# Performance work log

Measured on AMD Instinct MI355X. Metric: run time of the kernel, lower is better.

Reference implementation:

```python
import jax, jax.numpy as jnp
import numpy as np
import math

EMBED_DIM = 1024
N_HEAD = 16
HEAD_DIM = EMBED_DIM // N_HEAD


def setup_inputs() -> dict:
    key = jax.random.key(0)
    ks = jax.random.split(key, 9)
    B, T, C = 4, 2048, EMBED_DIM
    s = 1.0 / math.sqrt(C)
    return {
        "x": jax.random.normal(ks[0], (B, T, C), dtype=jnp.float32),
        "Wq": jax.random.normal(ks[1], (C, C), dtype=jnp.float32) * s,
        "bq": jnp.zeros((C,), dtype=jnp.float32),
        "Wk": jax.random.normal(ks[2], (C, C), dtype=jnp.float32) * s,
        "bk": jnp.zeros((C,), dtype=jnp.float32),
        "Wv": jax.random.normal(ks[3], (C, C), dtype=jnp.float32) * s,
        "bv": jnp.zeros((C,), dtype=jnp.float32),
        "Wp": jax.random.normal(ks[4], (C, C), dtype=jnp.float32) * s,
        "bp": jnp.zeros((C,), dtype=jnp.float32),
    }


def reference(x, Wq, bq, Wk, bk, Wv, bv, Wp, bp):
    B, T, C = x.shape
    H, D = N_HEAD, HEAD_DIM

    def heads(W, b):
        # [B,T,C] -> [B,H,T,D]
        return (x @ W.T + b).reshape(B, T, H, D).transpose(0, 2, 1, 3)

    q = heads(Wq, bq)
    k = heads(Wk, bk)
    v = heads(Wv, bv)

    att = jnp.einsum("bhtd,bhsd->bhts", q, k) * (1.0 / math.sqrt(D))
    causal = jnp.tril(jnp.ones((T, T), dtype=bool))
    att = jnp.where(causal[None, None], att, -jnp.inf)
    att = jax.nn.softmax(att, axis=-1)
    y = jnp.einsum("bhts,bhsd->bhtd", att, v)  # [B,H,T,D]
    y = y.transpose(0, 2, 1, 3).reshape(B, T, C)
    return y @ Wp.T + bp
```

## Files before the change

### kernel.cpp

```cpp
#include <hip/hip_runtime.h>
#include <hip/hip_bf16.h>
#include <cstdint>
#include <cstddef>

#define TQ 2048
#define CDIM 1024
#define NH 16
#define HD 64

typedef __attribute__((ext_vector_type(8))) short bf16x8;
typedef __attribute__((ext_vector_type(4))) float f32x4;
typedef __attribute__((ext_vector_type(16))) float f32x16;

__device__ __forceinline__ unsigned short f2bf(float f) {
  union { float f; unsigned u; } x; x.f = f;
  unsigned r = x.u + 0x7fffu + ((x.u >> 16) & 1u);
  return (unsigned short)(r >> 16);
}

__device__ __forceinline__ unsigned cvtpk(float lo, float hi) {
  unsigned r;
  asm("v_cvt_pk_bf16_f32 %0, %1, %2" : "=v"(r) : "v"(lo), "v"(hi));
  return r;
}

__device__ __forceinline__ void plswap(unsigned& x, unsigned& y) {
  asm("v_permlane32_swap_b32 %0, %1" : "+v"(x), "+v"(y));
}

__device__ __forceinline__ float exp2_fast(float x) {
  float r;
  asm("v_exp_f32 %0, %1" : "=v"(r) : "v"(x));
  return r;
}

__device__ __forceinline__ void gload_lds16(const void* g, void* l) {
  typedef __attribute__((address_space(1))) const void gv;
  typedef __attribute__((address_space(3))) void lv;
  __builtin_amdgcn_global_load_lds((gv*)g, (lv*)l, 16, 0, 0);
}

#define BAR() do { asm volatile("" ::: "memory"); __builtin_amdgcn_s_barrier(); asm volatile("" ::: "memory"); } while (0)
#define VMC2() asm volatile("s_waitcnt vmcnt(2)" ::: "memory")
#define VMC0() asm volatile("s_waitcnt vmcnt(0)" ::: "memory")

__global__ void cvt_bf16_kernel(const float* __restrict__ in,
                                unsigned short* __restrict__ out, int n) {
  int stride = gridDim.x * blockDim.x;
  for (int i = blockIdx.x * blockDim.x + threadIdx.x; i * 4 < n; i += stride) {
    float4 v = *(const float4*)(in + (size_t)i * 4);
    ushort4 o;
    o.x = f2bf(v.x); o.y = f2bf(v.y); o.z = f2bf(v.z); o.w = f2bf(v.w);
    *(ushort4*)(out + (size_t)i * 4) = o;
  }
}

__global__ void cvt4_kernel(const float* __restrict__ w0, const float* __restrict__ w1,
                            const float* __restrict__ w2, const float* __restrict__ w3,
                            unsigned short* __restrict__ out) {
  int i = blockIdx.x * blockDim.x + threadIdx.x;
  int which = i >> 18;
  const float* src = which == 0 ? w0 : which == 1 ? w1 : which == 2 ? w2 : w3;
  int off = (i & 262143) * 4;
  float4 v = *(const float4*)(src + off);
  ushort4 o;
  o.x = f2bf(v.x); o.y = f2bf(v.y); o.z = f2bf(v.z); o.w = f2bf(v.w);
  *(ushort4*)(out + (size_t)i * 4) = o;
}

template <int EPI>
__global__ __launch_bounds__(512, 2) void gemm256_kernel(
    const unsigned short* __restrict__ A,
    const unsigned short* __restrict__ Bt,
    const float* __restrict__ b0, const float* __restrict__ b1,
    void* __restrict__ outp,
    int M, int N, int K) {
  __shared__ __align__(16) char lds[131072];

  const int tid = (int)threadIdx.x;
  const int w = tid >> 6, lane = tid & 63;
  const int g = lane >> 4, c = lane & 15;
  const int wm = w >> 2, wn = w & 3;

  const int nbm = M >> 8, nbn = N >> 8;
  const int nwg = nbm * nbn;
  int id = (int)blockIdx.x;
  const int cpx = nwg >> 3;
  id = (id & 7) * cpx + (id >> 3);
  const int tm = id % nbm, tn = id / nbm;

  const char* Ab = (const char*)(A + (size_t)tm * 256 * K);
  const char* Bb = (const char*)(Bt + (size_t)tn * 256 * K);
  const int rowB = K * 2;
  const int nht = (K >> 6) << 2;

  char* aw = lds + wm * 16384;
  char* bw = lds + 65536 + (wn >> 1) * 16384;
  const int bfo = (wn & 1) * 8;

  auto stage_ht = [&](int j) {
    if (j >= nht) return;
    const int t = j >> 2, part = j & 3;
    const int isB = part >> 1, half = part & 1;
    const char* src = isB ? Bb : Ab;
    char* dst = lds + isB * 65536 + (t & 1) * 32768 + half * 16384 + w * 2048;
#pragma unroll
    for (int r = 0; r < 2; ++r) {
      const int f = w * 2 + r;
      const int m16 = f >> 1, ki = f & 1;
      gload_lds16(src + (size_t)(half * 128 + m16 * 16 + c) * rowB +
                      t * 128 + ki * 64 + g * 16,
                  dst + r * 1024);
    }
  };

  f32x4 acc[8][4];
#pragma unroll
  for (int i = 0; i < 8; ++i)
#pragma unroll
    for (int j = 0; j < 4; ++j) acc[i][j] = (f32x4){0.f, 0.f, 0.f, 0.f};
  bf16x8 af[4][2], bv[2][2];

  auto rdA = [&](int buf, int ms) {
#pragma unroll
    for (int mi = 0; mi < 4; ++mi)
#pragma unroll
      for (int ki = 0; ki < 2; ++ki)
        af[mi][ki] = *(const bf16x8*)(aw + buf * 32768 +
                                      ((ms * 4 + mi) * 2 + ki) * 1024 + lane * 16);
  };
  auto rdB = [&](int buf, int ns) {
#pragma unroll
    for (int ni = 0; ni < 2; ++ni)
#pragma unroll
      for (int ki = 0; ki < 2; ++ki)
        bv[ni][ki] = *(const bf16x8*)(bw + buf * 32768 +
                                      (bfo + (ns * 2 + ni) * 2 + ki) * 1024 + lane * 16);
  };
  auto mm = [&](int ms, int ns) {
    __builtin_amdgcn_s_setprio(1);
#pragma unroll
    for (int mi = 0; mi < 4; ++mi)
#pragma unroll
      for (int ni = 0; ni < 2; ++ni)
#pragma unroll
        for (int ki = 0; ki < 2; ++ki)
          acc[ms * 4 + mi][ns * 2 + ni] = __builtin_amdgcn_mfma_f32_16x16x32_bf16(
              af[mi][ki], bv[ni][ki], acc[ms * 4 + mi][ns * 2 + ni], 0, 0, 0);
    __builtin_amdgcn_s_setprio(0);
  };

  for (int j = 0; j < 5; ++j) stage_ht(j);
  VMC2();
  BAR();

  const int niter = K >> 7;
#pragma unroll 1
  for (int i = 0; i < niter; ++i) {
    const int j0 = 5 + (i << 3);
    rdA(0, 0); rdB(0, 0); stage_ht(j0 + 0); BAR(); mm(0, 0); BAR();
    rdB(0, 1);            stage_ht(j0 + 1); BAR(); mm(0, 1); BAR();
    rdA(0, 1);            stage_ht(j0 + 2); BAR(); mm(1, 1); BAR();
    rdB(0, 0);            stage_ht(j0 + 3);
    if (i + 1 < niter) { VMC2(); } else { VMC0(); }
    BAR(); mm(1, 0); BAR();
    rdA(1, 0); rdB(1, 0); stage_ht(j0 + 4); BAR(); mm(0, 0); BAR();
    rdB(1, 1);            stage_ht(j0 + 5); BAR(); mm(0, 1); BAR();
    rdA(1, 1);            stage_ht(j0 + 6); BAR(); mm(1, 1); BAR();
    rdB(1, 0);            stage_ht(j0 + 7); VMC2(); BAR(); mm(1, 0); BAR();
  }

#pragma unroll
  for (int mi = 0; mi < 8; ++mi) {
#pragma unroll
    for (int ni = 0; ni < 4; ++ni) {
      const int n = tn * 256 + wn * 64 + ni * 16 + c;
#pragma unroll
      for (int e = 0; e < 4; ++e) {
        const int m = tm * 256 + wm * 128 + mi * 16 + g * 4 + e;
        float v = acc[mi][ni][e];
        if (EPI == 4) {
          unsigned short* O = (unsigned short*)outp;
          if (n < 1024) {
            v = (v + b0[n]) * 0.18033688f;
            size_t idx = ((size_t)(m >> 11) * NH + (n >> 6)) * (TQ * HD) +
                         (size_t)(m & (TQ - 1)) * HD + (n & (HD - 1));
            O[idx] = f2bf(v);
          } else {
            int nn = n - 1024;
            v += b1[nn];
            size_t idx = 8388608 + ((size_t)(m >> 11) * NH + (nn >> 6)) * (TQ * HD) +
                         (size_t)(m & (TQ - 1)) * HD + (nn & (HD - 1));
            O[idx] = f2bf(v);
          }
        }
      }
    }
  }
}

template <int EPI>
__global__ __launch_bounds__(512, 2) void gemm128x256_kernel(
    const unsigned short* __restrict__ A,
    const unsigned short* __restrict__ Bt,
    const float* __restrict__ b0, const float* __restrict__ b1,
    void* __restrict__ outp,
    int M, int N, int K) {
  __shared__ __align__(16) char lds[98304];

  const int tid = (int)threadIdx.x;
  const int w = tid >> 6, lane = tid & 63;
  const int g = lane >> 4, c = lane & 15;
  const int wm = w >> 2, wn = w & 3;

  const int nbm = M >> 7, nbn = N >> 8;
  const int nwg = nbm * nbn;
  int id = (int)blockIdx.x;
  const int cpx = nwg >> 3;
  id = (id & 7) * cpx + (id >> 3);
  const int tm = id % nbm, tn = id / nbm;

  const char* Ab = (const char*)(A + (size_t)tm * 128 * K);
  const char* Bb = (const char*)(Bt + (size_t)tn * 256 * K);
  const int rowB = K * 2;
  const int nt = K >> 6;

  auto stageA = [&](int t) {
    if (t >= nt) return;
    char* dst = lds + (t & 1) * 49152 + (w << 11);
    const char* s = Ab + (size_t)(w * 16 + c) * rowB + t * 128 + g * 16;
    gload_lds16(s, dst);
    gload_lds16(s + 64, dst + 1024);
  };
  auto stageB = [&](int t, int odd) {
    if (t >= nt) return;
    const int n16 = (w >> 1) * 4 + 2 * odd + (w & 1);
    char* dst = lds + (t & 1) * 49152 + 16384 + (n16 << 11);
    const char* s = Bb + (size_t)(n16 * 16 + c) * rowB + t * 128 + g * 16;
    gload_lds16(s, dst);
    gload_lds16(s + 64, dst + 1024);
  };

  f32x4 acc[4][4];
#pragma unroll
  for (int i = 0; i < 4; ++i)
#pragma unroll
    for (int j = 0; j < 4; ++j) acc[i][j] = (f32x4){0.f, 0.f, 0.f, 0.f};
  bf16x8 af[2][2], bv[2][2][2];

  auto rdA = [&](int cur, int ms) {
#pragma unroll
    for (int mi2 = 0; mi2 < 2; ++mi2)
#pragma unroll
      for (int ki = 0; ki < 2; ++ki)
        af[mi2][ki] = *(const bf16x8*)(lds + cur * 49152 +
            (((wm * 4 + ms * 2 + mi2) << 1) + ki) * 1024 + lane * 16);
  };
  auto rdB = [&](int cur, int ns) {
#pragma unroll
    for (int ni2 = 0; ni2 < 2; ++ni2)
#pragma unroll
      for (int ki = 0; ki < 2; ++ki)
        bv[ns][ni2][ki] = *(const bf16x8*)(lds + cur * 49152 + 16384 +
            (((wn * 4 + ns * 2 + ni2) << 1) + ki) * 1024 + lane * 16);
  };
  auto mm = [&](int ms, int ns) {
    __builtin_amdgcn_s_setprio(1);
#pragma unroll
    for (int mi2 = 0; mi2 < 2; ++mi2)
#pragma unroll
      for (int ni2 = 0; ni2 < 2; ++ni2)
#pragma unroll
        for (int ki = 0; ki < 2; ++ki)
          acc[ms * 2 + mi2][ns * 2 + ni2] = __builtin_amdgcn_mfma_f32_16x16x32_bf16(
              af[mi2][ki], bv[ns][ni2][ki], acc[ms * 2 + mi2][ns * 2 + ni2], 0, 0, 0);
    __builtin_amdgcn_s_setprio(0);
  };

  stageA(0); stageB(0, 0); stageB(0, 1);
  VMC2();
  BAR();

#pragma unroll 1
  for (int i = 0; i < (nt >> 1); ++i) {
    const int t0 = 2 * i, t1 = 2 * i + 1;
    rdA(0, 0); rdB(0, 0); stageA(t0 + 1);
    mm(0, 0); VMC2(); BAR();
    rdB(0, 1); stageB(t0 + 1, 0);
    mm(0, 1); BAR();
    rdA(0, 1); stageB(t0 + 1, 1);
    mm(1, 1); BAR();
    mm(1, 0); VMC2(); BAR();
    rdA(1, 0); rdB(1, 0); stageA(t1 + 1);
    mm(0, 0);
    if (t1 == nt - 1) { VMC0(); } else { VMC2(); }
    BAR();
    rdB(1, 1); stageB(t1 + 1, 0);
    mm(0, 1); BAR();
    rdA(1, 1); stageB(t1 + 1, 1);
    mm(1, 1); BAR();
    mm(1, 0); VMC2(); BAR();
  }

#pragma unroll
  for (int mi = 0; mi < 4; ++mi) {
#pragma unroll
    for (int ni = 0; ni < 4; ++ni) {
      const int n = tn * 256 + wn * 64 + ni * 16 + c;
#pragma unroll
      for (int e = 0; e < 4; ++e) {
        const int m = tm * 128 + wm * 64 + mi * 16 + g * 4 + e;
        float v = acc[mi][ni][e];
        if (EPI == 1) {
          v += b0[m];
          size_t idx = ((size_t)(n >> 11) * (NH * HD) + m) * TQ + (n & (TQ - 1));
          ((unsigned short*)outp)[idx] = f2bf(v);
        } else if (EPI == 2) {
          v += b0[n];
          ((float*)outp)[(size_t)m * N + n] = v;
        }
      }
    }
  }
}

__global__ __launch_bounds__(256, 4) void attn_kernel(
    const unsigned short* __restrict__ Q,
    const unsigned short* __restrict__ K,
    const unsigned short* __restrict__ Vt,
    unsigned short* __restrict__ Y) {
  __shared__ __align__(16) char Ks[2][8192];
  __shared__ __align__(16) char Vs[2][8192];

  const int tid = (int)threadIdx.x;
  const int w = tid >> 6, lane = tid & 63;
  const int l31 = lane & 31, hi = lane >> 5;

  const int n = (int)blockIdx.x;
  const int g = n & 255, k = n >> 8;
  const int bh = g >> 2;
  const int u = 2 * (g & 3) + (k >> 1);
  const int qt = (k & 1) ? (15 - u) : u;
  const int b = bh >> 4, h = bh & 15;

  const unsigned short* Qb = Q + (size_t)bh * TQ * HD;
  const char* Kb = (const char*)(K + (size_t)bh * TQ * HD);
  const char* Vb = (const char*)(Vt + (size_t)bh * HD * TQ);

  auto stage = [&](int buf, int kt) {
#pragma unroll
    for (int i = 0; i < 2; ++i) {
      const int s = i * 256 + tid;
      const int r32 = (s >> 8) * 32 + (s & 31);
      const int ck = ((s >> 6) & 3) * 32 + ((s >> 5) & 1) * 16;
      char* kdst = &Ks[buf][0] + i * 4096 + (w << 10);
      char* vdst = &Vs[buf][0] + i * 4096 + (w << 10);
      gload_lds16(Kb + (size_t)kt * 8192 + r32 * 128 + ck, kdst);
      gload_lds16(Vb + (size_t)r32 * 4096 + kt * 128 + ck, vdst);
    }
  };

  const int q0 = qt * 128 + w * 32;
  const int qg = q0 + l31;
  const int nkv = 2 * qt + 2;

  stage(0, 0);

  bf16x8 qf[4];
#pragma unroll
  for (int dk = 0; dk < 4; ++dk)
    qf[dk] = *(const bf16x8*)(Qb + (size_t)qg * HD + dk * 16 + hi * 8);

  f32x16 oac[2];
#pragma unroll
  for (int nb = 0; nb < 2; ++nb)
#pragma unroll
    for (int r = 0; r < 16; ++r) oac[nb][r] = 0.f;
  float mr = -3.0e38f, lr = 0.f;

  __syncthreads();

  for (int kt = 0; kt < nkv; ++kt) {
    const int cur = kt & 1;
    if (kt + 1 < nkv) stage(cur ^ 1, kt + 1);

    if (kt * 64 <= q0 + 31) {
      const char* Klane = &Ks[cur][0] + lane * 16;
      const char* Vlane = &Vs[cur][0] + lane * 16;

      f32x16 s0, s1;
#pragma unroll
      for (int r = 0; r < 16; ++r) { s0[r] = 0.f; s1[r] = 0.f; }
#pragma unroll
      for (int dk = 0; dk < 4; ++dk) {
        bf16x8 kf0 = *(const bf16x8*)(Klane + (dk << 10));
        bf16x8 kf1 = *(const bf16x8*)(Klane + ((4 + dk) << 10));
        s0 = __builtin_amdgcn_mfma_f32_32x32x16_bf16(kf0, qf[dk], s0, 0, 0, 0);
        s1 = __builtin_amdgcn_mfma_f32_32x32x16_bf16(kf1, qf[dk], s1, 0, 0, 0);
      }

      const bool maskT = (kt * 64 + 63 > q0);
      if (maskT) {
#pragma unroll
        for (int r = 0; r < 16; ++r) {
          int kv0 = kt * 64 + ((r & 3) + 8 * (r >> 2)) + 4 * hi;
          s0[r] = (kv0 <= qg) ? s0[r] : -3.0e38f;
          s1[r] = (kv0 + 32 <= qg) ? s1[r] : -3.0e38f;
        }
      }

      float mt_ = s0[0];
#pragma unroll
      for (int r = 1; r < 16; ++r) mt_ = fmaxf(mt_, s0[r]);
#pragma unroll
      for (int r = 0; r < 16; ++r) mt_ = fmaxf(mt_, s1[r]);
      mt_ = fmaxf(mt_, __shfl_xor(mt_, 32));

      if (!__all(mt_ - mr <= 8.0f)) {
        const float mn = fmaxf(mr, mt_);
        const float al = exp2_fast(mr - mn);
        mr = mn;
        lr *= al;
#pragma unroll
        for (int nb = 0; nb < 2; ++nb)
#pragma unroll
          for (int r = 0; r < 16; ++r) oac[nb][r] *= al;
      }

      float rs = 0.f;
#pragma unroll
      for (int r = 0; r < 16; ++r) { s0[r] = exp2_fast(s0[r] - mr); rs += s0[r]; }
#pragma unroll
      for (int r = 0; r < 16; ++r) { s1[r] = exp2_fast(s1[r] - mr); rs += s1[r]; }
      rs += __shfl_xor(rs, 32);
      lr += rs;

      bf16x8 pf[4];
      {
        unsigned a0 = cvtpk(s0[0], s0[1]), b0 = cvtpk(s0[2], s0[3]);
        unsigned c0 = cvtpk(s0[4], s0[5]), d0 = cvtpk(s0[6], s0[7]);
        plswap(a0, c0); plswap(b0, d0);
        unsigned a1 = cvtpk(s0[8], s0[9]), b1 = cvtpk(s0[10], s0[11]);
        unsigned c1 = cvtpk(s0[12], s0[13]), d1 = cvtpk(s0[14], s0[15]);
        plswap(a1, c1); plswap(b1, d1);
        unsigned a2 = cvtpk(s1[0], s1[1]), b2 = cvtpk(s1[2], s1[3]);
        unsigned c2 = cvtpk(s1[4], s1[5]), d2 = cvtpk(s1[6], s1[7]);
        plswap(a2, c2); plswap(b2, d2);
        unsigned a3 = cvtpk(s1[8], s1[9]), b3 = cvtpk(s1[10], s1[11]);
        unsigned c3 = cvtpk(s1[12], s1[13]), d3 = cvtpk(s1[14], s1[15]);
        plswap(a3, c3); plswap(b3, d3);
        union { unsigned u[4]; bf16x8 v; } t;
        t.u[0] = a0; t.u[1] = b0; t.u[2] = c0; t.u[3] = d0; pf[0] = t.v;
        t.u[0] = a1; t.u[1] = b1; t.u[2] = c1; t.u[3] = d1; pf[1] = t.v;
        t.u[0] = a2; t.u[1] = b2; t.u[2] = c2; t.u[3] = d2; pf[2] = t.v;
        t.u[0] = a3; t.u[1] = b3; t.u[2] = c3; t.u[3] = d3; pf[3] = t.v;
      }

#pragma unroll
      for (int nb = 0; nb < 2; ++nb)
#pragma unroll
        for (int ks = 0; ks < 4; ++ks) {
          bf16x8 vf = *(const bf16x8*)(Vlane + (((nb << 2) + ks) << 10));
          oac[nb] = __builtin_amdgcn_mfma_f32_32x32x16_bf16(vf, pf[ks], oac[nb], 0, 0, 0);
        }
    }
    __syncthreads();
  }

  float inv;
  asm("v_rcp_f32 %0, %1" : "=v"(inv) : "v"(lr));
  unsigned short* Yrow = Y + (size_t)(b * TQ + qg) * CDIM + h * 64;
#pragma unroll
  for (int nb = 0; nb < 2; ++nb)
#pragma unroll
    for (int j = 0; j < 8; ++j) {
      const int dbase = ((2 * j) & 3) + 8 * (j >> 1);
      unsigned lo = f2bf(oac[nb][2 * j] * inv);
      unsigned hi2 = f2bf(oac[nb][2 * j + 1] * inv);
      *(unsigned*)(Yrow + nb * 32 + dbase + 4 * hi) = lo | (hi2 << 16);
    }
}

extern "C" void kernel_launch(void* const* d_in, const int* in_sizes, int n_in,
                              void* d_out, int out_size, void* d_ws, size_t ws_size,
                              hipStream_t stream) {
  (void)in_sizes; (void)n_in; (void)out_size; (void)ws_size;
  const float* x  = (const float*)d_in[0];
  const float* Wq = (const float*)d_in[1];
  const float* bq = (const float*)d_in[2];
  const float* Wk = (const float*)d_in[3];
  const float* bk = (const float*)d_in[4];
  const float* Wv = (const float*)d_in[5];
  const float* bv = (const float*)d_in[6];
  const float* Wp = (const float*)d_in[7];
  const float* bp = (const float*)d_in[8];
  float* out = (float*)d_out;

  char* ws = (char*)d_ws;
  unsigned short* xb  = (unsigned short*)(ws + 0);
  unsigned short* wqb = (unsigned short*)(ws + 16777216);
  unsigned short* wvb = (unsigned short*)(ws + 20971520);
  unsigned short* wpb = (unsigned short*)(ws + 23068672);
  unsigned short* Qh  = (unsigned short*)(ws + 25165824);
  unsigned short* Kh  = (unsigned short*)(ws + 41943040);
  unsigned short* Vt  = (unsigned short*)(ws + 58720256);
  unsigned short* y   = (unsigned short*)(ws + 75497472);

  const int nx = 4 * TQ * CDIM;

  cvt_bf16_kernel<<<4096, 256, 0, stream>>>(x, xb, nx);
  cvt4_kernel<<<4096, 256, 0, stream>>>(Wq, Wk, Wv, Wp, wqb);

  gemm256_kernel<4><<<256, 512, 0, stream>>>(xb, wqb, bq, bk, Qh, 8192, 2048, 1024);
  gemm128x256_kernel<1><<<256, 512, 0, stream>>>(wvb, xb, bv, bv, Vt, 1024, 8192, 1024);

  attn_kernel<<<1024, 256, 0, stream>>>(Qh, Kh, Vt, y);

  gemm128x256_kernel<2><<<256, 512, 0, stream>>>(y, wpb, bp, bp, out, 8192, 1024, 1024);
}
```

Before: 199.1 us.

## Merge conversion kernels, reorder GEMM tile mapping, tune attention softmax reductions

Combines the input and weight bf16 conversion kernels into one launch to save a kernel launch. Changes the workgroup-to-tile mapping in the QK GEMM and the output projection GEMM to row-major order for better L2 reuse. In attention, raises wave priority around MFMA blocks, and replaces the serial max and sum reductions with v_max3-based and pairwise tree reductions to shorten dependency chains. These are several independent micro-optimizations, and the priority hints and tile-order changes may help or hurt depending on scheduling.

```diff
diff --git a/kernel.cpp b/kernel.cpp
--- a/kernel.cpp
+++ b/kernel.cpp
@@ -34,6 +34,12 @@
   return r;
 }
 
+__device__ __forceinline__ float fmax3(float a, float b, float c) {
+  float r;
+  asm("v_max3_f32 %0, %1, %2, %3" : "=v"(r) : "v"(a), "v"(b), "v"(c));
+  return r;
+}
+
 __device__ __forceinline__ void gload_lds16(const void* g, void* l) {
   typedef __attribute__((address_space(1))) const void gv;
   typedef __attribute__((address_space(3))) void lv;
@@ -44,28 +50,29 @@
 #define VMC2() asm volatile("s_waitcnt vmcnt(2)" ::: "memory")
 #define VMC0() asm volatile("s_waitcnt vmcnt(0)" ::: "memory")
 
-__global__ void cvt_bf16_kernel(const float* __restrict__ in,
-                                unsigned short* __restrict__ out, int n) {
-  int stride = gridDim.x * blockDim.x;
-  for (int i = blockIdx.x * blockDim.x + threadIdx.x; i * 4 < n; i += stride) {
-    float4 v = *(const float4*)(in + (size_t)i * 4);
+__global__ void cvt_all_kernel(const float* __restrict__ x,
+                               const float* __restrict__ w0, const float* __restrict__ w1,
+                               const float* __restrict__ w2, const float* __restrict__ w3,
+                               unsigned short* __restrict__ xb,
+                               unsigned short* __restrict__ wb) {
+  const int bid = (int)blockIdx.x;
+  if (bid < 4096) {
+    for (int i = bid * 256 + threadIdx.x; i < 2097152; i += 4096 * 256) {
+      float4 v = *(const float4*)(x + (size_t)i * 4);
+      ushort4 o;
+      o.x = f2bf(v.x); o.y = f2bf(v.y); o.z = f2bf(v.z); o.w = f2bf(v.w);
+      *(ushort4*)(xb + (size_t)i * 4) = o;
+    }
+  } else {
+    int i = (bid - 4096) * 256 + threadIdx.x;
+    int which = i >> 18;
+    const float* src = which == 0 ? w0 : which == 1 ? w1 : which == 2 ? w2 : w3;
+    int off = (i & 262143) * 4;
+    float4 v = *(const float4*)(src + off);
     ushort4 o;
     o.x = f2bf(v.x); o.y = f2bf(v.y); o.z = f2bf(v.z); o.w = f2bf(v.w);
-    *(ushort4*)(out + (size_t)i * 4) = o;
+    *(ushort4*)(wb + (size_t)i * 4) = o;
   }
-}
-
-__global__ void cvt4_kernel(const float* __restrict__ w0, const float* __restrict__ w1,
-                            const float* __restrict__ w2, const float* __restrict__ w3,
-                            unsigned short* __restrict__ out) {
-  int i = blockIdx.x * blockDim.x + threadIdx.x;
-  int which = i >> 18;
-  const float* src = which == 0 ? w0 : which == 1 ? w1 : which == 2 ? w2 : w3;
-  int off = (i & 262143) * 4;
-  float4 v = *(const float4*)(src + off);
-  ushort4 o;
-  o.x = f2bf(v.x); o.y = f2bf(v.y); o.z = f2bf(v.z); o.w = f2bf(v.w);
-  *(ushort4*)(out + (size_t)i * 4) = o;
 }
 
 template <int EPI>
@@ -87,7 +94,7 @@
   int id = (int)blockIdx.x;
   const int cpx = nwg >> 3;
   id = (id & 7) * cpx + (id >> 3);
-  const int tm = id % nbm, tn = id / nbm;
+  const int tn = id % nbn, tm = id / nbn;
 
   const char* Ab = (const char*)(A + (size_t)tm * 256 * K);
   const char* Bb = (const char*)(Bt + (size_t)tn * 256 * K);
@@ -199,7 +206,7 @@
   }
 }
 
-template <int EPI>
+template <int EPI, int ROWMAJ>
 __global__ __launch_bounds__(512, 2) void gemm128x256_kernel(
     const unsigned short* __restrict__ A,
     const unsigned short* __restrict__ Bt,
@@ -218,7 +225,8 @@
   int id = (int)blockIdx.x;
   const int cpx = nwg >> 3;
   id = (id & 7) * cpx + (id >> 3);
-  const int tm = id % nbm, tn = id / nbm;
+  const int tm = ROWMAJ ? (id / nbn) : (id % nbm);
+  const int tn = ROWMAJ ? (id % nbn) : (id / nbm);
 
   const char* Ab = (const char*)(A + (size_t)tm * 128 * K);
   const char* Bb = (const char*)(Bt + (size_t)tn * 256 * K);
@@ -391,6 +399,7 @@
       f32x16 s0, s1;
 #pragma unroll
       for (int r = 0; r < 16; ++r) { s0[r] = 0.f; s1[r] = 0.f; }
+      __builtin_amdgcn_s_setprio(1);
 #pragma unroll
       for (int dk = 0; dk < 4; ++dk) {
         bf16x8 kf0 = *(const bf16x8*)(Klane + (dk << 10));
@@ -398,6 +407,7 @@
         s0 = __builtin_amdgcn_mfma_f32_32x32x16_bf16(kf0, qf[dk], s0, 0, 0, 0);
         s1 = __builtin_amdgcn_mfma_f32_32x32x16_bf16(kf1, qf[dk], s1, 0, 0, 0);
       }
+      __builtin_amdgcn_s_setprio(0);
 
       const bool maskT = (kt * 64 + 63 > q0);
       if (maskT) {
@@ -409,11 +419,22 @@
         }
       }
 
-      float mt_ = s0[0];
-#pragma unroll
-      for (int r = 1; r < 16; ++r) mt_ = fmaxf(mt_, s0[r]);
-#pragma unroll
-      for (int r = 0; r < 16; ++r) mt_ = fmaxf(mt_, s1[r]);
+      float m0 = fmax3(s0[0], s0[1], s0[2]);
+      float m1 = fmax3(s0[3], s0[4], s0[5]);
+      float m2 = fmax3(s0[6], s0[7], s0[8]);
+      float m3 = fmax3(s0[9], s0[10], s0[11]);
+      float m4 = fmax3(s0[12], s0[13], s0[14]);
+      float m5 = fmax3(s0[15], s1[0], s1[1]);
+      float m6 = fmax3(s1[2], s1[3], s1[4]);
+      float m7 = fmax3(s1[5], s1[6], s1[7]);
+      float m8 = fmax3(s1[8], s1[9], s1[10]);
+      float m9 = fmax3(s1[11], s1[12], s1[13]);
+      float ma = fmaxf(s1[14], s1[15]);
+      float n0 = fmax3(m0, m1, m2);
+      float n1 = fmax3(m3, m4, m5);
+      float n2 = fmax3(m6, m7, m8);
+      float n3 = fmax3(m9, ma, n0);
+      float mt_ = fmax3(n1, n2, n3);
       mt_ = fmaxf(mt_, __shfl_xor(mt_, 32));
 
       if (!__all(mt_ - mr <= 8.0f)) {
@@ -427,11 +448,21 @@
           for (int r = 0; r < 16; ++r) oac[nb][r] *= al;
       }
 
-      float rs = 0.f;
-#pragma unroll
-      for (int r = 0; r < 16; ++r) { s0[r] = exp2_fast(s0[r] - mr); rs += s0[r]; }
-#pragma unroll
-      for (int r = 0; r < 16; ++r) { s1[r] = exp2_fast(s1[r] - mr); rs += s1[r]; }
+#pragma unroll
+      for (int r = 0; r < 16; ++r) s0[r] = exp2_fast(s0[r] - mr);
+#pragma unroll
+      for (int r = 0; r < 16; ++r) s1[r] = exp2_fast(s1[r] - mr);
+      float rs;
+      {
+        float a0 = s0[0] + s0[1], a1 = s0[2] + s0[3], a2 = s0[4] + s0[5], a3 = s0[6] + s0[7];
+        float a4 = s0[8] + s0[9], a5 = s0[10] + s0[11], a6 = s0[12] + s0[13], a7 = s0[14] + s0[15];
+        float b0_ = s1[0] + s1[1], b1_ = s1[2] + s1[3], b2_ = s1[4] + s1[5], b3_ = s1[6] + s1[7];
+        float b4 = s1[8] + s1[9], b5 = s1[10] + s1[11], b6 = s1[12] + s1[13], b7 = s1[14] + s1[15];
+        float c0 = a0 + a1, c1 = a2 + a3, c2 = a4 + a5, c3 = a6 + a7;
+        float c4 = b0_ + b1_, c5 = b2_ + b3_, c6 = b4 + b5, c7 = b6 + b7;
+        float d0 = c0 + c1, d1 = c2 + c3, d2 = c4 + c5, d3 = c6 + c7;
+        rs = (d0 + d1) + (d2 + d3);
+      }
       rs += __shfl_xor(rs, 32);
       lr += rs;
 
@@ -456,6 +487,7 @@
         t.u[0] = a3; t.u[1] = b3; t.u[2] = c3; t.u[3] = d3; pf[3] = t.v;
       }
 
+      __builtin_amdgcn_s_setprio(1);
 #pragma unroll
       for (int nb = 0; nb < 2; ++nb)
 #pragma unroll
@@ -463,6 +495,7 @@
           bf16x8 vf = *(const bf16x8*)(Vlane + (((nb << 2) + ks) << 10));
           oac[nb] = __builtin_amdgcn_mfma_f32_32x32x16_bf16(vf, pf[ks], oac[nb], 0, 0, 0);
         }
+      __builtin_amdgcn_s_setprio(0);
     }
     __syncthreads();
   }
@@ -506,15 +539,12 @@
   unsigned short* Vt  = (unsigned short*)(ws + 58720256);
   unsigned short* y   = (unsigned short*)(ws + 75497472);
 
-  const int nx = 4 * TQ * CDIM;
-
-  cvt_bf16_kernel<<<4096, 256, 0, stream>>>(x, xb, nx);
-  cvt4_kernel<<<4096, 256, 0, stream>>>(Wq, Wk, Wv, Wp, wqb);
+  cvt_all_kernel<<<8192, 256, 0, stream>>>(x, Wq, Wk, Wv, Wp, xb, wqb);
 
   gemm256_kernel<4><<<256, 512, 0, stream>>>(xb, wqb, bq, bk, Qh, 8192, 2048, 1024);
-  gemm128x256_kernel<1><<<256, 512, 0, stream>>>(wvb, xb, bv, bv, Vt, 1024, 8192, 1024);
+  gemm128x256_kernel<1, 0><<<256, 512, 0, stream>>>(wvb, xb, bv, bv, Vt, 1024, 8192, 1024);
 
   attn_kernel<<<1024, 256, 0, stream>>>(Qh, Kh, Vt, y);
 
-  gemm128x256_kernel<2><<<256, 512, 0, stream>>>(y, wpb, bp, bp, out, 8192, 1024, 1024);
-}
+  gemm128x256_kernel<2, 1><<<256, 512, 0, stream>>>(y, wpb, bp, bp, out, 8192, 1024, 1024);
+}
```

After: 198.3 us. About the same (-0.4%).
